# Performance work log

Measured on AMD Instinct MI355X. Metric: run time of the kernel, lower is better.

## Reference

```python
import jax, jax.numpy as jnp
import numpy as np

TOP_K = 2


def setup_inputs() -> dict:
    key = jax.random.key(0)
    ks = jax.random.split(key, 6)
    B, S, H, I, E = 4, 2048, 1024, 4096, 8
    x = jax.random.normal(ks[0], (B, S, H), dtype=jnp.float32)
    Wr = jax.random.normal(ks[1], (H, E), dtype=jnp.float32) * (1.0 / np.sqrt(H))
    W1 = jax.random.normal(ks[2], (E, H, I), dtype=jnp.float32) * (1.0 / np.sqrt(H))
    b1 = jnp.zeros((E, I), dtype=jnp.float32)
    W2 = jax.random.normal(ks[3], (E, I, H), dtype=jnp.float32) * (1.0 / np.sqrt(I))
    b2 = jnp.zeros((E, H), dtype=jnp.float32)
    return {"x": x, "Wr": Wr, "W1": W1, "b1": b1, "W2": W2, "b2": b2}


def reference(x, Wr, W1, b1, W2, b2):
    B, S, H = x.shape
    E = Wr.shape[1]
    xf = x.reshape(-1, H)                              # [T, H], T = B*S
    logits = xf @ Wr                                   # [T, E]
    probs = jax.nn.softmax(logits, axis=-1)
    rw, sel = jax.lax.top_k(probs, TOP_K)              # [T, K]
    rw = rw / jnp.sum(rw, axis=-1, keepdims=True)
    out = jnp.zeros_like(xf)
    # Loop over small fixed expert count; each token contributes only via its
    # top-k combine weight (zero weight == not routed, matching index_add).
    for i in range(E):
        wi = jnp.sum(jnp.where(sel == i, rw, 0.0), axis=-1)    # [T]
        h = jax.nn.silu(xf @ W1[i] + b1[i])                    # [T, I]
        out = out + (h @ W2[i] + b2[i]) * wi[:, None]
    return out.reshape(B, S, H)
```

## Files before the change

kernel.cpp:

```cpp
#include <hip/hip_runtime.h>
#include <cstdint>
#include <cstddef>

#define TTOK 8192
#define HDIM 1024
#define IDIM 4096
#define NEXP 8
#define PMAX 18432
#define WS_NEED 302260352ULL

#define SLOT1 24576
#define SLOT2 16384

typedef __attribute__((ext_vector_type(8))) short bf16x8;
typedef __attribute__((ext_vector_type(4))) float f32x4;

#define AS3 __attribute__((address_space(3)))
#define AS1 __attribute__((address_space(1)))

__device__ __forceinline__ void gld16(const void* g, void* s) {
  __builtin_amdgcn_global_load_lds((const AS1 void*)g, (AS3 void*)s, 16, 0, 0);
}

__device__ __forceinline__ void pinned_barrier() {
  __builtin_amdgcn_sched_barrier(0);
  __builtin_amdgcn_s_barrier();
  __builtin_amdgcn_sched_barrier(0);
}

__device__ __forceinline__ unsigned short f2b(float f) {
  unsigned u = __builtin_bit_cast(unsigned, f);
  unsigned r = ((u >> 16) & 1u) + 0x7FFFu;
  return (unsigned short)((u + r) >> 16);
}

__device__ __forceinline__ float b2f(unsigned short u) {
  return __builtin_bit_cast(float, ((unsigned)u) << 16);
}


__device__ __forceinline__ void router_body(
    int bid, int t, const float* __restrict__ x, const float* __restrict__ wr,
    unsigned short* __restrict__ xb, int* __restrict__ t2e,
    float* __restrict__ t2w)
{
  const int tok = bid * 4 + (t >> 6);
  const int l = t & 63;
  const float* xr = x + (size_t)tok * HDIM;
  float acc[8] = {0.f,0.f,0.f,0.f,0.f,0.f,0.f,0.f};
  #pragma unroll
  for (int j = 0; j < 4; ++j) {
    const int base = j * 256 + l * 4;
    const float4 xv = *(const float4*)(xr + base);
    const float xa[4] = {xv.x, xv.y, xv.z, xv.w};
    ushort4 ub;
    ub.x = f2b(xa[0]); ub.y = f2b(xa[1]); ub.z = f2b(xa[2]); ub.w = f2b(xa[3]);
    *(ushort4*)(xb + (size_t)tok * HDIM + base) = ub;
    #pragma unroll
    for (int ii = 0; ii < 4; ++ii) {
      const float4 w0 = *(const float4*)(wr + (size_t)(base + ii) * 8);
      const float4 w1 = *(const float4*)(wr + (size_t)(base + ii) * 8 + 4);
      acc[0] += xa[ii] * w0.x; acc[1] += xa[ii] * w0.y;
      acc[2] += xa[ii] * w0.z; acc[3] += xa[ii] * w0.w;
      acc[4] += xa[ii] * w1.x; acc[5] += xa[ii] * w1.y;
      acc[6] += xa[ii] * w1.z; acc[7] += xa[ii] * w1.w;
    }
  }
  #pragma unroll
  for (int e = 0; e < 8; ++e) {
    float v = acc[e];
    #pragma unroll
    for (int off = 32; off > 0; off >>= 1) v += __shfl_xor(v, off);
    acc[e] = v;
  }
  if (l == 0) {
    float l0 = -1e30f; int i0 = 0;
    #pragma unroll
    for (int e = 0; e < 8; ++e) if (acc[e] > l0) { l0 = acc[e]; i0 = e; }
    float l1 = -1e30f; int i1 = (i0 == 0) ? 1 : 0;
    #pragma unroll
    for (int e = 0; e < 8; ++e) if (e != i0 && acc[e] > l1) { l1 = acc[e]; i1 = e; }
    const float w0 = 1.f / (1.f + expf(l1 - l0));
    t2e[tok * 2] = i0; t2e[tok * 2 + 1] = i1;
    t2w[tok * 2] = w0; t2w[tok * 2 + 1] = 1.f - w0;
  }
}

__device__ __forceinline__ void packT_body(
    int bid, int t, uint32_t* __restrict__ plds,
    const float* __restrict__ src, unsigned short* __restrict__ dst,
    int K, int N)
{
  const int tiles_n = N >> 8, tiles_k = K >> 5;
  const int e = bid / (tiles_k * tiles_n);
  const int rem = bid % (tiles_k * tiles_n);
  const int kt = rem / tiles_n, it = rem % tiles_n;
  const float* S = src + (size_t)e * K * N + (size_t)kt * 32 * N + (size_t)it * 256;
  unsigned short* D = dst + (size_t)e * N * K + (size_t)it * 256 * K + (size_t)kt * 32;
  #pragma unroll
  for (int q = 0; q < 4; ++q) {
    const int task = q * 256 + t;
    const int i4 = task & 63, kp = task >> 6;
    const float* p0 = S + (size_t)(2 * kp) * N + i4 * 4;
    const float4 r0 = *(const float4*)p0;
    const float4 r1 = *(const float4*)(p0 + N);
    const float a0[4] = {r0.x, r0.y, r0.z, r0.w};
    const float a1[4] = {r1.x, r1.y, r1.z, r1.w};
    #pragma unroll
    for (int j = 0; j < 4; ++j)
      plds[(i4 * 4 + j) * 17 + kp] = (uint32_t)f2b(a0[j]) | ((uint32_t)f2b(a1[j]) << 16);
  }
  __syncthreads();
  #pragma unroll
  for (int r = 0; r < 4; ++r) {
    const int idx = r * 256 + t;
    const int il = idx >> 2, q4 = idx & 3;
    uint4 o;
    o.x = plds[il * 17 + q4 * 4 + 0];
    o.y = plds[il * 17 + q4 * 4 + 1];
    o.z = plds[il * 17 + q4 * 4 + 2];
    o.w = plds[il * 17 + q4 * 4 + 3];
    *(uint4*)(D + (size_t)il * K + q4 * 8) = o;
  }
}

__global__ __launch_bounds__(256, 2) void prep_k(
    const float* __restrict__ x, const float* __restrict__ wr,
    unsigned short* __restrict__ xb, int* __restrict__ t2e,
    float* __restrict__ t2w,
    const float* __restrict__ w1, unsigned short* __restrict__ w1t,
    const float* __restrict__ w2, unsigned short* __restrict__ w2t)
{
  __shared__ uint32_t plds[256 * 17];
  const int bid = blockIdx.x, t = threadIdx.x;
  if (bid < 2048) {
    router_body(bid, t, x, wr, xb, t2e, t2w);
  } else if (bid < 2048 + 4096) {
    packT_body(bid - 2048, t, plds, w1, w1t, HDIM, IDIM);
  } else {
    packT_body(bid - 6144, t, plds, w2, w2t, IDIM, HDIM);
  }
}

__global__ void count_k(const int* __restrict__ t2e, int* __restrict__ meta) {
  const int t = threadIdx.x, w = t >> 6, l = t & 63;
  int cnt[8] = {0,0,0,0,0,0,0,0};
  for (int c = 0; c < 16; ++c) {
    const int tok = (w * 16 + c) * 64 + l;
    const int e0 = t2e[2 * tok], e1 = t2e[2 * tok + 1];
    #pragma unroll
    for (int e = 0; e < 8; ++e)
      cnt[e] += __popcll(__ballot(e0 == e)) + __popcll(__ballot(e1 == e));
  }
  __shared__ int part[8][8];
  if (l == 0) {
    #pragma unroll
    for (int e = 0; e < 8; ++e) part[w][e] = cnt[e];
  }
  __syncthreads();
  if (t == 0) {
    int off = 0;
    #pragma unroll
    for (int e = 0; e < 8; ++e) {
      int s = 0;
      #pragma unroll
      for (int w2 = 0; w2 < 8; ++w2) s += part[w2][e];
      meta[e] = s; meta[16 + e] = off; off += (s + 255) & ~255;
    }
    meta[24] = off;
  }
}

__global__ void scatter_k(const int* __restrict__ t2e, const int* __restrict__ meta,
                          int* __restrict__ ltok, int* __restrict__ t2p)
{
  const int e = blockIdx.x;
  const int t = threadIdx.x, w = t >> 6, l = t & 63;
  const int off = meta[16 + e];
  const int cnt = meta[e];
  __shared__ int wsum[4];
  __shared__ int base;
  if (t == 0) base = 0;
  __syncthreads();
  const unsigned long long lt = (1ULL << l) - 1ULL;
  for (int c = 0; c < TTOK / 256; ++c) {
    const int tok = c * 256 + t;
    const bool m0 = (t2e[2 * tok] == e);
    const bool m1 = (t2e[2 * tok + 1] == e);
    const unsigned long long b0 = __ballot(m0);
    const unsigned long long b1 = __ballot(m1);
    const int n0 = __popcll(b0), n1 = __popcll(b1);
    const int r0 = __popcll(b0 & lt);
    const int r1 = n0 + __popcll(b1 & lt);
    if (l == 0) wsum[w] = n0 + n1;
    __syncthreads();
    int wb = base;
    #pragma unroll
    for (int i = 0; i < 4; ++i) if (i < w) wb += wsum[i];
    const int tot = wsum[0] + wsum[1] + wsum[2] + wsum[3];
    __syncthreads();
    if (t == 0) base += tot;
    if (m0) { const int p = off + wb + r0; ltok[p] = tok; t2p[2 * tok] = p; }
    if (m1) { const int p = off + wb + r1; ltok[p] = tok; t2p[2 * tok + 1] = p; }
    __syncthreads();
  }
  const int padded = (cnt + 255) & ~255;
  for (int i = cnt + t; i < padded; i += 256) ltok[off + i] = -1;
}


__global__ __launch_bounds__(512, 4) void gemm1_k(
    const unsigned short* __restrict__ xb, const unsigned short* __restrict__ w1t,
    const float* __restrict__ b1, const int* __restrict__ meta,
    const int* __restrict__ ltok, unsigned short* __restrict__ h)
{
  const int wg = blockIdx.x;
  const int id = (wg & 7) * (2304 / 8) + (wg >> 3);
  const int mt = id >> 5, nt = id & 31;
  if (mt * 256 >= meta[24]) return;
  int e = 0;
  #pragma unroll
  for (int i = 1; i < 8; ++i) if (meta[16 + i] <= mt * 256) e = i;

  extern __shared__ char lds[];
  const int t = threadIdx.x;
  const int w = t >> 6, l = t & 63;
  const int wn = w & 1, wm = w >> 1;

  const unsigned short* asrc;
  {
    const int G = t;
    const int line = G >> 3, q = (G & 7) ^ (line & 7);
    const int row = 2 * line + (q >> 2), g = q & 3;
    asrc = w1t + ((size_t)e * IDIM + nt * 128 + row) * HDIM + g * 8;
  }
  const unsigned short* bsrc[2];
  #pragma unroll
  for (int c = 0; c < 2; ++c) {
    const int G = c * 512 + t;
    const int line = G >> 3, q = (G & 7) ^ (line & 7);
    const int row = 2 * line + (q >> 2), g = q & 3;
    int tok = ltok[mt * 256 + row]; if (tok < 0) tok = 0;
    bsrc[c] = xb + (size_t)tok * HDIM + g * 8;
  }

  const int lr = l & 15, lg = l >> 4;
  f32x4 acc[4][4] = {};

  auto STAGE = [&](int kt) {
    char* sb = lds + (kt % 3) * SLOT1;
    const int ks = kt * 32;
    gld16(asrc + ks, sb + w * 1024);
    gld16(bsrc[0] + ks, sb + 8192 + w * 1024);
    gld16(bsrc[1] + ks, sb + 16384 + w * 1024);
  };

  STAGE(0); STAGE(1);
  const int NT = HDIM / 32;
  for (int kt = 0; kt < NT; ++kt) {
    if (kt + 1 < NT) {
      asm volatile("s_waitcnt vmcnt(3)" ::: "memory");
    } else {
      asm volatile("s_waitcnt vmcnt(0)" ::: "memory");
    }
    pinned_barrier();
    const char* sl = lds + (kt % 3) * SLOT1;
    bf16x8 af[4], bf[4];
    #pragma unroll
    for (int f = 0; f < 4; ++f) {
      const int rowA = wn * 64 + f * 16 + lr;
      const int lineA = rowA >> 1;
      const int pA = (((rowA & 1) << 2) + lg) ^ (lineA & 7);
      af[f] = *(const bf16x8*)(sl + lineA * 128 + pA * 16);
      const int rowB = wm * 64 + f * 16 + lr;
      const int lineB = rowB >> 1;
      const int pB = (((rowB & 1) << 2) + lg) ^ (lineB & 7);
      bf[f] = *(const bf16x8*)(sl + 8192 + lineB * 128 + pB * 16);
    }
    if (kt + 2 < NT) STAGE(kt + 2);
    __builtin_amdgcn_s_setprio(1);
    #pragma unroll
    for (int fm = 0; fm < 4; ++fm)
      #pragma unroll
      for (int fn = 0; fn < 4; ++fn)
        acc[fm][fn] = __builtin_amdgcn_mfma_f32_16x16x32_bf16(af[fm], bf[fn], acc[fm][fn], 0, 0, 0);
    __builtin_amdgcn_s_setprio(0);
    pinned_barrier();
  }

  const int lg4 = lg * 4;
  #pragma unroll
  for (int fm = 0; fm < 4; ++fm) {
    const int ib = nt * 128 + wn * 64 + fm * 16 + lg4;
    const float4 b1v = *(const float4*)(b1 + e * IDIM + ib);
    #pragma unroll
    for (int fn = 0; fn < 4; ++fn) {
      const int trow = mt * 256 + wm * 64 + fn * 16 + lr;
      const float v0 = acc[fm][fn][0] + b1v.x;
      const float v1 = acc[fm][fn][1] + b1v.y;
      const float v2 = acc[fm][fn][2] + b1v.z;
      const float v3 = acc[fm][fn][3] + b1v.w;
      ushort4 st;
      st.x = f2b(v0 / (1.f + __expf(-v0)));
      st.y = f2b(v1 / (1.f + __expf(-v1)));
      st.z = f2b(v2 / (1.f + __expf(-v2)));
      st.w = f2b(v3 / (1.f + __expf(-v3)));
      *(ushort4*)(h + (size_t)trow * IDIM + ib) = st;
    }
  }
}

__global__ __launch_bounds__(256, 3) void gemm2_k(
    const unsigned short* __restrict__ h, const unsigned short* __restrict__ w2t,
    const int* __restrict__ meta, unsigned short* __restrict__ y)
{
  const int wg = blockIdx.x;
  const int id = (wg & 7) * (1152 / 8) + (wg >> 3);
  const int mt = id >> 3, nt = id & 7;
  if (mt * 128 >= meta[24]) return;
  int e = 0;
  #pragma unroll
  for (int i = 1; i < 8; ++i) if (meta[16 + i] <= mt * 128) e = i;

  extern __shared__ char lds[];
  const int t = threadIdx.x;
  const int w = t >> 6, l = t & 63;
  const int wn = w & 1, wm = w >> 1;

  const unsigned short* asrc[2]; const unsigned short* bsrc[2];
  #pragma unroll
  for (int c = 0; c < 2; ++c) {
    const int G = c * 256 + t;
    const int line = G >> 3, q = (G & 7) ^ (line & 7);
    const int row = 2 * line + (q >> 2), g = q & 3;
    asrc[c] = w2t + ((size_t)e * HDIM + nt * 128 + row) * IDIM + g * 8;
    bsrc[c] = h + (size_t)(mt * 128 + row) * IDIM + g * 8;
  }

  const int lr = l & 15, lg = l >> 4;
  f32x4 acc[4][4] = {};

  auto STAGE = [&](int kt) {
    char* sb = lds + (kt % 3) * SLOT2;
    const int ks = kt * 32;
    gld16(asrc[0] + ks, sb + w * 1024);
    gld16(asrc[1] + ks, sb + 4096 + w * 1024);
    gld16(bsrc[0] + ks, sb + 8192 + w * 1024);
    gld16(bsrc[1] + ks, sb + 12288 + w * 1024);
  };

  STAGE(0); STAGE(1);
  const int NT = IDIM / 32;
  for (int kt = 0; kt < NT; ++kt) {
    if (kt + 1 < NT) {
      asm volatile("s_waitcnt vmcnt(4)" ::: "memory");
    } else {
      asm volatile("s_waitcnt vmcnt(0)" ::: "memory");
    }
    pinned_barrier();
    const char* sl = lds + (kt % 3) * SLOT2;
    bf16x8 af[4], bf[4];
    #pragma unroll
    for (int f = 0; f < 4; ++f) {
      const int rowA = wn * 64 + f * 16 + lr;
      const int lineA = rowA >> 1;
      const int pA = (((rowA & 1) << 2) + lg) ^ (lineA & 7);
      af[f] = *(const bf16x8*)(sl + lineA * 128 + pA * 16);
      const int rowB = wm * 64 + f * 16 + lr;
      const int lineB = rowB >> 1;
      const int pB = (((rowB & 1) << 2) + lg) ^ (lineB & 7);
      bf[f] = *(const bf16x8*)(sl + 8192 + lineB * 128 + pB * 16);
    }
    if (kt + 2 < NT) STAGE(kt + 2);
    __builtin_amdgcn_s_setprio(1);
    #pragma unroll
    for (int fm = 0; fm < 4; ++fm)
      #pragma unroll
      for (int fn = 0; fn < 4; ++fn)
        acc[fm][fn] = __builtin_amdgcn_mfma_f32_16x16x32_bf16(af[fm], bf[fn], acc[fm][fn], 0, 0, 0);
    __builtin_amdgcn_s_setprio(0);
    pinned_barrier();
  }

  const int lg4 = lg * 4;
  #pragma unroll
  for (int fm = 0; fm < 4; ++fm) {
    const int colb = nt * 128 + wn * 64 + fm * 16 + lg4;
    #pragma unroll
    for (int fn = 0; fn < 4; ++fn) {
      const int row = mt * 128 + wm * 64 + fn * 16 + lr;
      ushort4 st;
      st.x = f2b(acc[fm][fn][0]); st.y = f2b(acc[fm][fn][1]);
      st.z = f2b(acc[fm][fn][2]); st.w = f2b(acc[fm][fn][3]);
      *(ushort4*)(y + (size_t)row * HDIM + colb) = st;
    }
  }
}

__global__ __launch_bounds__(256, 4) void combine_k(
    const unsigned short* __restrict__ y, const float* __restrict__ b2,
    const int* __restrict__ t2e, const float* __restrict__ t2w,
    const int* __restrict__ t2p, float* __restrict__ out)
{
  const int t = blockIdx.x * 4 + (threadIdx.x >> 6);
  const int l = threadIdx.x & 63;
  const int e0 = t2e[t * 2], e1 = t2e[t * 2 + 1];
  const float w0 = t2w[t * 2], w1v = t2w[t * 2 + 1];
  const int p0 = t2p[t * 2], p1 = t2p[t * 2 + 1];
  const unsigned short* y0 = y + (size_t)p0 * HDIM;
  const unsigned short* y1 = y + (size_t)p1 * HDIM;
  const float* bb0 = b2 + e0 * HDIM;
  const float* bb1 = b2 + e1 * HDIM;
  float* o = out + (size_t)t * HDIM;
  #pragma unroll
  for (int j = 0; j < 4; ++j) {
    const int c = j * 256 + l * 4;
    const ushort4 a = *(const ushort4*)(y0 + c);
    const ushort4 b = *(const ushort4*)(y1 + c);
    const float4 c0 = *(const float4*)(bb0 + c);
    const float4 c1 = *(const float4*)(bb1 + c);
    float4 r;
    r.x = w0 * (b2f(a.x) + c0.x) + w1v * (b2f(b.x) + c1.x);
    r.y = w0 * (b2f(a.y) + c0.y) + w1v * (b2f(b.y) + c1.y);
    r.z = w0 * (b2f(a.z) + c0.z) + w1v * (b2f(b.z) + c1.z);
    r.w = w0 * (b2f(a.w) + c0.w) + w1v * (b2f(b.w) + c1.w);
    *(float4*)(o + c) = r;
  }
}

__global__ void sentinel_k(float* out) { out[0] = 1.0e6f; }

extern "C" void kernel_launch(void* const* d_in, const int* in_sizes, int n_in,
                              void* d_out, int out_size, void* d_ws, size_t ws_size,
                              hipStream_t stream)
{
  (void)in_sizes; (void)n_in; (void)out_size;
  const float* x  = (const float*)d_in[0];
  const float* wr = (const float*)d_in[1];
  const float* w1 = (const float*)d_in[2];
  const float* b1 = (const float*)d_in[3];
  const float* w2 = (const float*)d_in[4];
  const float* b2 = (const float*)d_in[5];
  float* out = (float*)d_out;
  char* ws = (char*)d_ws;

  if (ws_size < WS_NEED) { sentinel_k<<<1, 1, 0, stream>>>(out); return; }

  unsigned short* xb  = (unsigned short*)(ws);
  unsigned short* w1t = (unsigned short*)(ws + 16777216);
  unsigned short* w2t = (unsigned short*)(ws + 83886080);
  unsigned short* h   = (unsigned short*)(ws + 150994944);
  int*   t2e  = (int*)(ws + 301989888);
  float* t2w  = (float*)(ws + 302055424);
  int*   ltok = (int*)(ws + 302120960);
  int*   t2p  = (int*)(ws + 302194688);
  int*   meta = (int*)(ws + 302260224);
  unsigned short* y = (unsigned short*)(ws);

  hipFuncSetAttribute((const void*)gemm1_k, hipFuncAttributeMaxDynamicSharedMemorySize, 3 * SLOT1);
  hipFuncSetAttribute((const void*)gemm2_k, hipFuncAttributeMaxDynamicSharedMemorySize, 3 * SLOT2);

  prep_k<<<10240, 256, 0, stream>>>(x, wr, xb, t2e, t2w, w1, w1t, w2, w2t);
  count_k<<<1, 512, 0, stream>>>(t2e, meta);
  scatter_k<<<NEXP, 256, 0, stream>>>(t2e, meta, ltok, t2p);

  gemm1_k<<<72 * 32, 512, 3 * SLOT1, stream>>>(xb, w1t, b1, meta, ltok, h);
  gemm2_k<<<144 * 8, 256, 3 * SLOT2, stream>>>(h, w2t, meta, y);
  combine_k<<<TTOK / 4, 256, 0, stream>>>(y, b2, t2e, t2w, t2p, out);
}
```

Before: 532.6 us.

## Split gemm2 along K into two halves and fold count into scatter

gemm2 now runs twice as many workgroups, each handling half of the intermediate dimension. Each half writes its own bf16 partial output buffer, and combine_k adds the two partials before applying bias and routing weights. This is meant to improve wave balance and occupancy across CUs, at the cost of extra partial-output traffic and rounding each partial to bf16. Separately, the single-block count kernel is merged into scatter_k: every expert block recounts all tokens and computes its own offset, which removes one launch but repeats the counting work in each block.

```diff
diff --git a/kernel.cpp b/kernel.cpp
--- a/kernel.cpp
+++ b/kernel.cpp
@@ -142,42 +142,45 @@
   }
 }
 
-__global__ void count_k(const int* __restrict__ t2e, int* __restrict__ meta) {
+__global__ void scatter_k(const int* __restrict__ t2e, int* __restrict__ meta,
+                          int* __restrict__ ltok, int* __restrict__ t2p)
+{
+  const int e = blockIdx.x;
   const int t = threadIdx.x, w = t >> 6, l = t & 63;
-  int cnt[8] = {0,0,0,0,0,0,0,0};
-  for (int c = 0; c < 16; ++c) {
-    const int tok = (w * 16 + c) * 64 + l;
-    const int e0 = t2e[2 * tok], e1 = t2e[2 * tok + 1];
-    #pragma unroll
-    for (int e = 0; e < 8; ++e)
-      cnt[e] += __popcll(__ballot(e0 == e)) + __popcll(__ballot(e1 == e));
-  }
-  __shared__ int part[8][8];
-  if (l == 0) {
-    #pragma unroll
-    for (int e = 0; e < 8; ++e) part[w][e] = cnt[e];
+  __shared__ int part[4][8];
+  __shared__ int soff, scnt;
+  {
+    int cnt[8] = {0,0,0,0,0,0,0,0};
+    for (int c = 0; c < 32; ++c) {
+      const int tok = (w * 32 + c) * 64 + l;
+      const int e0 = t2e[2 * tok], e1 = t2e[2 * tok + 1];
+      #pragma unroll
+      for (int i = 0; i < 8; ++i)
+        cnt[i] += __popcll(__ballot(e0 == i)) + __popcll(__ballot(e1 == i));
+    }
+    if (l == 0) {
+      #pragma unroll
+      for (int i = 0; i < 8; ++i) part[w][i] = cnt[i];
+    }
   }
   __syncthreads();
   if (t == 0) {
-    int off = 0;
-    #pragma unroll
-    for (int e = 0; e < 8; ++e) {
-      int s = 0;
-      #pragma unroll
-      for (int w2 = 0; w2 < 8; ++w2) s += part[w2][e];
-      meta[e] = s; meta[16 + e] = off; off += (s + 255) & ~255;
-    }
-    meta[24] = off;
-  }
-}
-
-__global__ void scatter_k(const int* __restrict__ t2e, const int* __restrict__ meta,
-                          int* __restrict__ ltok, int* __restrict__ t2p)
-{
-  const int e = blockIdx.x;
-  const int t = threadIdx.x, w = t >> 6, l = t & 63;
-  const int off = meta[16 + e];
-  const int cnt = meta[e];
+    int off = 0, mycnt = 0, tot = 0;
+    #pragma unroll
+    for (int i = 0; i < 8; ++i) {
+      const int s = part[0][i] + part[1][i] + part[2][i] + part[3][i];
+      const int pad = (s + 255) & ~255;
+      if (i == e) mycnt = s;
+      if (i < e) off += pad;
+      tot += pad;
+    }
+    soff = off; scnt = mycnt;
+    meta[16 + e] = off;
+    if (e == 0) meta[24] = tot;
+  }
+  __syncthreads();
+  const int off = soff, cnt = scnt;
+
   __shared__ int wsum[4];
   __shared__ int base;
   if (t == 0) base = 0;
@@ -315,8 +318,8 @@
     const int* __restrict__ meta, unsigned short* __restrict__ y)
 {
   const int wg = blockIdx.x;
-  const int id = (wg & 7) * (1152 / 8) + (wg >> 3);
-  const int mt = id >> 3, nt = id & 7;
+  const int id = (wg & 7) * (2304 / 8) + (wg >> 3);
+  const int nt = id & 7, kh = (id >> 3) & 1, mt = id >> 4;
   if (mt * 128 >= meta[24]) return;
   int e = 0;
   #pragma unroll
@@ -326,6 +329,7 @@
   const int t = threadIdx.x;
   const int w = t >> 6, l = t & 63;
   const int wn = w & 1, wm = w >> 1;
+  const int kbase = kh * (IDIM / 2);
 
   const unsigned short* asrc[2]; const unsigned short* bsrc[2];
   #pragma unroll
@@ -333,8 +337,8 @@
     const int G = c * 256 + t;
     const int line = G >> 3, q = (G & 7) ^ (line & 7);
     const int row = 2 * line + (q >> 2), g = q & 3;
-    asrc[c] = w2t + ((size_t)e * HDIM + nt * 128 + row) * IDIM + g * 8;
-    bsrc[c] = h + (size_t)(mt * 128 + row) * IDIM + g * 8;
+    asrc[c] = w2t + ((size_t)e * HDIM + nt * 128 + row) * IDIM + kbase + g * 8;
+    bsrc[c] = h + (size_t)(mt * 128 + row) * IDIM + kbase + g * 8;
   }
 
   const int lr = l & 15, lg = l >> 4;
@@ -350,7 +354,7 @@
   };
 
   STAGE(0); STAGE(1);
-  const int NT = IDIM / 32;
+  const int NT = IDIM / 2 / 32;
   for (int kt = 0; kt < NT; ++kt) {
     if (kt + 1 < NT) {
       asm volatile("s_waitcnt vmcnt(4)" ::: "memory");
@@ -382,6 +386,7 @@
     pinned_barrier();
   }
 
+  unsigned short* yo = y + (size_t)kh * PMAX * HDIM;
   const int lg4 = lg * 4;
   #pragma unroll
   for (int fm = 0; fm < 4; ++fm) {
@@ -392,7 +397,7 @@
       ushort4 st;
       st.x = f2b(acc[fm][fn][0]); st.y = f2b(acc[fm][fn][1]);
       st.z = f2b(acc[fm][fn][2]); st.w = f2b(acc[fm][fn][3]);
-      *(ushort4*)(y + (size_t)row * HDIM + colb) = st;
+      *(ushort4*)(yo + (size_t)row * HDIM + colb) = st;
     }
   }
 }
@@ -407,23 +412,27 @@
   const int e0 = t2e[t * 2], e1 = t2e[t * 2 + 1];
   const float w0 = t2w[t * 2], w1v = t2w[t * 2 + 1];
   const int p0 = t2p[t * 2], p1 = t2p[t * 2 + 1];
-  const unsigned short* y0 = y + (size_t)p0 * HDIM;
-  const unsigned short* y1 = y + (size_t)p1 * HDIM;
+  const unsigned short* ya0 = y + (size_t)p0 * HDIM;
+  const unsigned short* yb0 = y + (size_t)PMAX * HDIM + (size_t)p0 * HDIM;
+  const unsigned short* ya1 = y + (size_t)p1 * HDIM;
+  const unsigned short* yb1 = y + (size_t)PMAX * HDIM + (size_t)p1 * HDIM;
   const float* bb0 = b2 + e0 * HDIM;
   const float* bb1 = b2 + e1 * HDIM;
   float* o = out + (size_t)t * HDIM;
   #pragma unroll
   for (int j = 0; j < 4; ++j) {
     const int c = j * 256 + l * 4;
-    const ushort4 a = *(const ushort4*)(y0 + c);
-    const ushort4 b = *(const ushort4*)(y1 + c);
+    const ushort4 a0 = *(const ushort4*)(ya0 + c);
+    const ushort4 a1 = *(const ushort4*)(yb0 + c);
+    const ushort4 b0v = *(const ushort4*)(ya1 + c);
+    const ushort4 b1u = *(const ushort4*)(yb1 + c);
     const float4 c0 = *(const float4*)(bb0 + c);
     const float4 c1 = *(const float4*)(bb1 + c);
     float4 r;
-    r.x = w0 * (b2f(a.x) + c0.x) + w1v * (b2f(b.x) + c1.x);
-    r.y = w0 * (b2f(a.y) + c0.y) + w1v * (b2f(b.y) + c1.y);
-    r.z = w0 * (b2f(a.z) + c0.z) + w1v * (b2f(b.z) + c1.z);
-    r.w = w0 * (b2f(a.w) + c0.w) + w1v * (b2f(b.w) + c1.w);
+    r.x = w0 * (b2f(a0.x) + b2f(a1.x) + c0.x) + w1v * (b2f(b0v.x) + b2f(b1u.x) + c1.x);
+    r.y = w0 * (b2f(a0.y) + b2f(a1.y) + c0.y) + w1v * (b2f(b0v.y) + b2f(b1u.y) + c1.y);
+    r.z = w0 * (b2f(a0.z) + b2f(a1.z) + c0.z) + w1v * (b2f(b0v.z) + b2f(b1u.z) + c1.z);
+    r.w = w0 * (b2f(a0.w) + b2f(a1.w) + c0.w) + w1v * (b2f(b0v.w) + b2f(b1u.w) + c1.w);
     *(float4*)(o + c) = r;
   }
 }
@@ -461,10 +470,9 @@
   hipFuncSetAttribute((const void*)gemm2_k, hipFuncAttributeMaxDynamicSharedMemorySize, 3 * SLOT2);
 
   prep_k<<<10240, 256, 0, stream>>>(x, wr, xb, t2e, t2w, w1, w1t, w2, w2t);
-  count_k<<<1, 512, 0, stream>>>(t2e, meta);
   scatter_k<<<NEXP, 256, 0, stream>>>(t2e, meta, ltok, t2p);
 
   gemm1_k<<<72 * 32, 512, 3 * SLOT1, stream>>>(xb, w1t, b1, meta, ltok, h);
-  gemm2_k<<<144 * 8, 256, 3 * SLOT2, stream>>>(h, w2t, meta, y);
+  gemm2_k<<<144 * 8 * 2, 256, 3 * SLOT2, stream>>>(h, w2t, meta, y);
   combine_k<<<TTOK / 4, 256, 0, stream>>>(y, b2, t2e, t2w, t2p, out);
 }
```

Measured after the change: 536.0 us. No clear change (+0.6%).
